# Optimization experiments

Hardware: AMD Instinct MI355X
Metric: run time of the kernel (lower is better)

Reference implementation:

```python
import jax, jax.numpy as jnp
import numpy as np

N, E = 50000, 400000          # nodes, edges
IN, H, OUT = 256, 512, 256    # channels
L, K = 2, 2                   # num_layers, Chebyshev order


def setup_inputs() -> dict:
    key = jax.random.key(0)
    ks = jax.random.split(key, 8)
    x = jax.random.normal(ks[0], (N, IN), jnp.float32)
    edge_index = jax.random.randint(ks[1], (2, E), 0, N)
    in_w = jax.random.normal(ks[2], (IN, H), jnp.float32) / np.float32(np.sqrt(IN))
    in_b = jnp.zeros((H,), jnp.float32)
    # ChebConv has K bias-free Linear layers per conv plus one bias vector
    conv_w = jax.random.normal(ks[3], (L, K, H, H), jnp.float32) / np.float32(np.sqrt(H))
    conv_b = jnp.zeros((L, H), jnp.float32)
    out_w = jax.random.normal(ks[4], (H, OUT), jnp.float32) / np.float32(np.sqrt(H))
    out_b = jnp.zeros((OUT,), jnp.float32)
    return dict(x=x, edge_index=edge_index, in_w=in_w, in_b=in_b,
                conv_w=conv_w, conv_b=conv_b, out_w=out_w, out_b=out_b)


def reference(x, edge_index, in_w, in_b, conv_w, conv_b, out_w, out_b):
    # PyG ChebConv normalization with lambda_max=2 (default):
    #   L_hat = 2/lambda_max * (I - D^{-1/2} A D^{-1/2}) - I = -D^{-1/2} A D^{-1/2}
    # i.e. off-diagonal weights -dinv[row]*w*dinv[col], diagonal 0.
    row, col = edge_index[0], edge_index[1]
    w = jnp.ones((E,), x.dtype)
    deg = jax.ops.segment_sum(w, row, num_segments=N)
    dinv = jnp.where(deg > 0, jax.lax.rsqrt(jnp.maximum(deg, 1e-12)), 0.0).astype(x.dtype)
    norm = -dinv[row] * w * dinv[col]  # [E]

    def prop(h):  # L_hat @ h  (gather from source row, scatter-add to target col)
        return jax.ops.segment_sum(norm[:, None] * h[row], col, num_segments=N)

    # dropout is identity in eval mode; reference is deterministic (eval)
    h = jax.nn.silu(x @ in_w + in_b)
    for l in range(L):
        # Chebyshev recursion, K=2: out = Tx0 @ W0 + (L_hat Tx0) @ W1 + b
        Tx0 = h
        out = Tx0 @ conv_w[l, 0]
        Tx1 = prop(Tx0)
        out = out + Tx1 @ conv_w[l, 1] + conv_b[l]
        h = jax.nn.silu(out)
    return h @ out_w + out_b
```

## Files before the change

kernel.cpp:

```cpp
#include <hip/hip_runtime.h>

#define H512 512

typedef short bf16x8 __attribute__((ext_vector_type(8)));
typedef float f32x4  __attribute__((ext_vector_type(4)));

__device__ __forceinline__ float silu_f(float v) { return v / (1.0f + __expf(-v)); }

__device__ __forceinline__ short f2bf(float f) {
    unsigned u = __float_as_uint(f);
    u = (u + 0x7FFFu + ((u >> 16) & 1u)) >> 16;
    return (short)u;
}
__device__ __forceinline__ float bf2f(short s) {
    return __uint_as_float(((unsigned)(unsigned short)s) << 16);
}


__global__ void hist_kernel(const int* __restrict__ row, const int* __restrict__ col,
                            float* __restrict__ deg, int* __restrict__ cnt, int E) {
    int e = blockIdx.x * blockDim.x + threadIdx.x;
    if (e < E) {
        atomicAdd(&deg[row[e]], 1.0f);
        atomicAdd(&cnt[col[e]], 1);
    }
}

__global__ void dinv_kernel(const float* __restrict__ deg, float* __restrict__ dinv, int n) {
    int i = blockIdx.x * blockDim.x + threadIdx.x;
    if (i < n) {
        float d = deg[i];
        dinv[i] = d > 0.0f ? rsqrtf(fmaxf(d, 1e-12f)) : 0.0f;
    }
}


__global__ __launch_bounds__(256) void bsum_kernel(const int* __restrict__ cnt,
                                                   int* __restrict__ bsum, int n) {
    __shared__ int s[4];
    int i = blockIdx.x * 256 + threadIdx.x;
    int v = (i < n) ? cnt[i] : 0;
    #pragma unroll
    for (int off = 32; off; off >>= 1) v += __shfl_down(v, off, 64);
    if ((threadIdx.x & 63) == 0) s[threadIdx.x >> 6] = v;
    __syncthreads();
    if (threadIdx.x == 0) bsum[blockIdx.x] = s[0] + s[1] + s[2] + s[3];
}

__global__ __launch_bounds__(256) void bscan_kernel(const int* __restrict__ bsum,
                                                    int* __restrict__ boff, int B) {
    __shared__ int s[256];
    int tid = threadIdx.x;
    int v = (tid < B) ? bsum[tid] : 0;
    s[tid] = v;
    __syncthreads();
    #pragma unroll
    for (int off = 1; off < 256; off <<= 1) {
        int t = (tid >= off) ? s[tid - off] : 0;
        __syncthreads();
        s[tid] += t;
        __syncthreads();
    }
    if (tid < B) boff[tid] = s[tid] - v;
}

__global__ __launch_bounds__(256) void cscan_kernel(const int* __restrict__ cnt,
                                                    const int* __restrict__ boff,
                                                    int* __restrict__ ptr,
                                                    int* __restrict__ ptr2, int n, int B) {
    __shared__ int s[256];
    int b = blockIdx.x, tid = threadIdx.x;
    int i = b * 256 + tid;
    int v = (i < n) ? cnt[i] : 0;
    s[tid] = v;
    __syncthreads();
    #pragma unroll
    for (int off = 1; off < 256; off <<= 1) {
        int t = (tid >= off) ? s[tid - off] : 0;
        __syncthreads();
        s[tid] += t;
        __syncthreads();
    }
    int exc = boff[b] + s[tid] - v;
    if (i < n) { ptr[i] = exc; ptr2[i] = exc; }
    if (b == B - 1 && tid == 255) ptr[n] = exc + v;
}

__global__ void scatter_kernel(const int* __restrict__ row, const int* __restrict__ col,
                               const float* __restrict__ dinv, int* __restrict__ ptr2,
                               int* __restrict__ esrc, float* __restrict__ ew, int E) {
    int e = blockIdx.x * blockDim.x + threadIdx.x;
    if (e >= E) return;
    int r = row[e], c = col[e];
    int pos = atomicAdd(&ptr2[c], 1);
    esrc[pos] = r;
    ew[pos]   = -dinv[r] * dinv[c];
}


__global__ void wt_kernel(const float* __restrict__ W, short* __restrict__ Wt, int K, int Nw) {
    int tid = blockIdx.x * blockDim.x + threadIdx.x;
    if (tid >= K * Nw) return;
    int n = tid / K, k = tid - n * K;
    Wt[(size_t)n * K + k] = f2bf(W[(size_t)k * Nw + n]);
}

__global__ void xconv_kernel(const float* __restrict__ x, short* __restrict__ xb,
                             int Nreal, int Mpad) {
    int tid = blockIdx.x * blockDim.x + threadIdx.x;
    if (tid >= Mpad * 32) return;
    int r = tid >> 5, c8 = (tid & 31) * 8;
    bf16x8 o = {0, 0, 0, 0, 0, 0, 0, 0};
    if (r < Nreal) {
        const float4 f0 = *(const float4*)(x + (size_t)r * 256 + c8);
        const float4 f1 = *(const float4*)(x + (size_t)r * 256 + c8 + 4);
        o[0] = f2bf(f0.x); o[1] = f2bf(f0.y); o[2] = f2bf(f0.z); o[3] = f2bf(f0.w);
        o[4] = f2bf(f1.x); o[5] = f2bf(f1.y); o[6] = f2bf(f1.z); o[7] = f2bf(f1.w);
    }
    *(bf16x8*)(xb + (size_t)r * 256 + c8) = o;
}


__global__ __launch_bounds__(256) void gather_kernel(
    const int* __restrict__ ptr, const int* __restrict__ esrc,
    const float* __restrict__ ew, const short* __restrict__ T,
    short* __restrict__ U, int N_)
{
    int t = threadIdx.x;
    int node = blockIdx.x * 4 + (t >> 6);
    if (node >= N_) return;
    int q = (t & 63) * 8;
    float acc[8] = {0.f, 0.f, 0.f, 0.f, 0.f, 0.f, 0.f, 0.f};
    const int i1 = ptr[node + 1];
    for (int i = ptr[node]; i < i1; ++i) {
        int s   = esrc[i];
        float w = ew[i];
        bf16x8 tv = *(const bf16x8*)(T + (size_t)s * H512 + q);
        #pragma unroll
        for (int j = 0; j < 8; ++j) acc[j] += w * bf2f(tv[j]);
    }
    bf16x8 o;
    #pragma unroll
    for (int j = 0; j < 8; ++j) o[j] = f2bf(acc[j]);
    *(bf16x8*)(U + (size_t)node * H512 + q) = o;
}


template<int ACCUM, int BIAS, int SILU, int F32OUT>
__global__ __launch_bounds__(256) void mfma_gemm(
    const short* __restrict__ A, int lda,
    const short* __restrict__ Bt, int ldb,
    const short* __restrict__ Cin, void* __restrict__ Cout, int ldc,
    const float* __restrict__ bias, int Mreal, int K)
{
    __shared__ alignas(16) short As[128 * 64];
    __shared__ alignas(16) short Bs[128 * 64];

    const int t    = threadIdx.x;
    const int lane = t & 63;
    const int wid  = t >> 6;
    const int m0   = blockIdx.y * 128;
    const int n0   = blockIdx.x * 128;
    const int wm   = wid >> 1;
    const int wn   = wid & 1;

    const int srow  = lane >> 3;
    const int scol  = (lane & 7) * 16;
    const int corig = scol ^ (srow << 4);
    const int cel   = corig >> 1;

    f32x4 acc[4][4];
    #pragma unroll
    for (int m = 0; m < 4; ++m)
        #pragma unroll
        for (int n = 0; n < 4; ++n)
            acc[m][n] = (f32x4){0.f, 0.f, 0.f, 0.f};

    const int r = lane & 15;
    const int g = lane >> 4;

    for (int k0 = 0; k0 < K; k0 += 64) {
        #pragma unroll
        for (int i = 0; i < 4; ++i) {
            const int r0 = (wid * 4 + i) * 8;
            const short* ga = A  + (size_t)(m0 + r0 + srow) * lda + (k0 + cel);
            __builtin_amdgcn_global_load_lds(
                (const __attribute__((address_space(1))) void*)ga,
                (__attribute__((address_space(3))) void*)(As + r0 * 64), 16, 0, 0);
            const short* gb = Bt + (size_t)(n0 + r0 + srow) * ldb + (k0 + cel);
            __builtin_amdgcn_global_load_lds(
                (const __attribute__((address_space(1))) void*)gb,
                (__attribute__((address_space(3))) void*)(Bs + r0 * 64), 16, 0, 0);
        }
        asm volatile("s_waitcnt vmcnt(0)" ::: "memory");
        __syncthreads();

        #pragma unroll
        for (int ks = 0; ks < 2; ++ks) {
            bf16x8 af[4], bfr[4];
            #pragma unroll
            for (int m = 0; m < 4; ++m) {
                const int rowA = wm * 64 + m * 16 + r;
                const int cb   = (ks * 64 + g * 16) ^ ((rowA & 7) << 4);
                af[m] = *(const bf16x8*)((const char*)As + rowA * 128 + cb);
            }
            #pragma unroll
            for (int n = 0; n < 4; ++n) {
                const int rowB = wn * 64 + n * 16 + r;
                const int cb   = (ks * 64 + g * 16) ^ ((rowB & 7) << 4);
                bfr[n] = *(const bf16x8*)((const char*)Bs + rowB * 128 + cb);
            }
            #pragma unroll
            for (int m = 0; m < 4; ++m)
                #pragma unroll
                for (int n = 0; n < 4; ++n)
                    acc[m][n] = __builtin_amdgcn_mfma_f32_16x16x32_bf16(
                        af[m], bfr[n], acc[m][n], 0, 0, 0);
        }
        __syncthreads();
    }

    #pragma unroll
    for (int n = 0; n < 4; ++n) {
        const int col = n0 + wn * 64 + n * 16 + r;
        float bb = 0.f;
        if (BIAS) bb = bias[col];
        #pragma unroll
        for (int m = 0; m < 4; ++m) {
            const int row0 = m0 + wm * 64 + m * 16 + g * 4;
            #pragma unroll
            for (int j = 0; j < 4; ++j) {
                const int rr = row0 + j;
                float v = acc[m][n][j];
                if (ACCUM) v += bf2f(Cin[(size_t)rr * ldc + col]);
                if (BIAS)  v += bb;
                if (SILU)  v = silu_f(v);
                if (F32OUT) {
                    if (rr < Mreal) ((float*)Cout)[(size_t)rr * ldc + col] = v;
                } else {
                    ((short*)Cout)[(size_t)rr * ldc + col] = f2bf(v);
                }
            }
        }
    }
}


extern "C" void kernel_launch(void* const* d_in, const int* in_sizes, int n_in,
                              void* d_out, int out_size, void* d_ws, size_t ws_size,
                              hipStream_t stream)
{
    const float* x      = (const float*)d_in[0];
    const int*   ei     = (const int*)  d_in[1];
    const float* in_w   = (const float*)d_in[2];
    const float* in_b   = (const float*)d_in[3];
    const float* conv_w = (const float*)d_in[4];
    const float* conv_b = (const float*)d_in[5];
    const float* out_w  = (const float*)d_in[6];
    const float* out_b  = (const float*)d_in[7];

    const int N = in_sizes[0] / 256;
    const int E = in_sizes[1] / 2;
    const int MPAD = ((N + 127) / 128) * 128;
    const int* row = ei;
    const int* col = ei + E;

    char* p = (char*)d_ws;
    short* h0 = (short*)p; p += (size_t)MPAD * H512 * 2;
    short* h1 = (short*)p; p += (size_t)MPAD * H512 * 2;
    short* T  = (short*)p; p += (size_t)MPAD * H512 * 2;
    short* U  = (short*)p; p += (size_t)MPAD * H512 * 2;
    short* xb = T;
    short* wti = (short*)p; p += (size_t)512 * 256 * 2;
    short* wtc = (short*)p; p += (size_t)4 * 512 * 512 * 2;
    short* wto = (short*)p; p += (size_t)256 * 512 * 2;
    float* deg  = (float*)p; p += (size_t)N * 4;
    float* dinv = (float*)p; p += (size_t)N * 4;
    float* ew   = (float*)p; p += (size_t)E * 4;
    int*   cnt  = (int*)p;   p += (size_t)N * 4;
    int*   ptr  = (int*)p;   p += (size_t)(N + 4) * 4;
    int*   ptr2 = (int*)p;   p += (size_t)N * 4;
    int*   esrc = (int*)p;   p += (size_t)E * 4;
    int*   bsum = (int*)p;   p += (size_t)256 * 4;
    int*   boff = (int*)p;   p += (size_t)256 * 4;

    const int NB = (N + 255) / 256;

    hipMemsetAsync(deg, 0, (size_t)N * sizeof(float), stream);
    hipMemsetAsync(cnt, 0, (size_t)N * sizeof(int), stream);
    hist_kernel<<<(E + 255) / 256, 256, 0, stream>>>(row, col, deg, cnt, E);
    dinv_kernel<<<(N + 255) / 256, 256, 0, stream>>>(deg, dinv, N);
    bsum_kernel <<<NB, 256, 0, stream>>>(cnt, bsum, N);
    bscan_kernel<<<1, 256, 0, stream>>>(bsum, boff, NB);
    cscan_kernel<<<NB, 256, 0, stream>>>(cnt, boff, ptr, ptr2, N, NB);
    scatter_kernel<<<(E + 255) / 256, 256, 0, stream>>>(row, col, dinv, ptr2, esrc, ew, E);

    wt_kernel<<<(256 * 512 + 255) / 256, 256, 0, stream>>>(in_w, wti, 256, 512);
    for (int i = 0; i < 4; ++i)
        wt_kernel<<<(512 * 512 + 255) / 256, 256, 0, stream>>>(
            conv_w + (size_t)i * 512 * 512, wtc + (size_t)i * 512 * 512, 512, 512);
    wt_kernel<<<(512 * 256 + 255) / 256, 256, 0, stream>>>(out_w, wto, 512, 256);
    xconv_kernel<<<(MPAD * 32 + 255) / 256, 256, 0, stream>>>(x, xb, N, MPAD);

    const int mt = MPAD / 128;

    mfma_gemm<0, 1, 1, 0><<<dim3(4, mt), 256, 0, stream>>>(
        xb, 256, wti, 256, nullptr, h0, H512, in_b, N, 256);

    short* hc = h0;
    short* hn = h1;
    for (int l = 0; l < 2; ++l) {
        mfma_gemm<0, 0, 0, 0><<<dim3(4, mt), 256, 0, stream>>>(
            hc, H512, wtc + (size_t)(l * 2 + 1) * 512 * 512, 512,
            nullptr, T, H512, nullptr, N, 512);
        gather_kernel<<<(N + 3) / 4, 256, 0, stream>>>(ptr, esrc, ew, T, U, N);
        mfma_gemm<1, 1, 1, 0><<<dim3(4, mt), 256, 0, stream>>>(
            hc, H512, wtc + (size_t)(l * 2 + 0) * 512 * 512, 512,
            U, hn, H512, conv_b + (size_t)l * H512, N, 512);
        short* tmp = hc; hc = hn; hn = tmp;
    }

    mfma_gemm<0, 1, 0, 1><<<dim3(2, mt), 256, 0, stream>>>(
        hc, H512, wto, 512, nullptr, d_out, 256, out_b, N, 512);
}
```

Measured before the change: 542.7 us.

## Stage GEMM epilogue through LDS for vectorized stores, swizzle blocks across XCDs

The GEMM epilogue now writes accumulators into a rotated LDS tile, then each thread handles a contiguous 32-column row segment. This lets Cin reads, bias loads and output stores use 16-byte vector accesses instead of scattered scalar ones. Workgroups are launched on a 1D grid and remapped so that neighbouring tiles land on the same XCD, aiming for better L2 reuse of the A and B panels. The weight transpose kernel also switches to an LDS-tiled, coalesced version. The cost is extra LDS traffic and two additional barriers per epilogue.

After: 576.2 us. 1.06x slower.

```diff
diff --git a/kernel.cpp b/kernel.cpp
--- a/kernel.cpp
+++ b/kernel.cpp
@@ -14,6 +14,14 @@
 }
 __device__ __forceinline__ float bf2f(short s) {
     return __uint_as_float(((unsigned)(unsigned short)s) << 16);
+}
+
+__device__ __forceinline__ int xcd_swz(int b, int nwg) {
+    const int NX = 8;
+    int q = nwg / NX, rr = nwg % NX;
+    int xcd = b % NX, idx = b / NX;
+    int base = (xcd < rr) ? xcd * (q + 1) : rr * (q + 1) + (xcd - rr) * q;
+    return base + idx;
 }
 
 
@@ -98,11 +106,25 @@
 }
 
 
-__global__ void wt_kernel(const float* __restrict__ W, short* __restrict__ Wt, int K, int Nw) {
-    int tid = blockIdx.x * blockDim.x + threadIdx.x;
-    if (tid >= K * Nw) return;
-    int n = tid / K, k = tid - n * K;
-    Wt[(size_t)n * K + k] = f2bf(W[(size_t)k * Nw + n]);
+__global__ __launch_bounds__(256) void wt_kernel(const float* __restrict__ W,
+                                                 short* __restrict__ Wt, int K, int Nw) {
+    __shared__ float tile[32][33];
+    const int tx = threadIdx.x & 31;
+    const int ty = threadIdx.x >> 5;
+    const int nt = Nw / 32;
+    const int k0 = (blockIdx.x / nt) * 32;
+    const int n0 = (blockIdx.x % nt) * 32;
+    #pragma unroll
+    for (int i = 0; i < 4; ++i) {
+        const int k = ty + i * 8;
+        tile[k][tx] = W[(size_t)(k0 + k) * Nw + n0 + tx];
+    }
+    __syncthreads();
+    #pragma unroll
+    for (int i = 0; i < 4; ++i) {
+        const int a = ty + i * 8;
+        Wt[(size_t)(n0 + a) * K + k0 + tx] = f2bf(tile[tx][a]);
+    }
 }
 
 __global__ void xconv_kernel(const float* __restrict__ x, short* __restrict__ xb,
@@ -151,16 +173,20 @@
     const short* __restrict__ A, int lda,
     const short* __restrict__ Bt, int ldb,
     const short* __restrict__ Cin, void* __restrict__ Cout, int ldc,
-    const float* __restrict__ bias, int Mreal, int K)
+    const float* __restrict__ bias, int Mreal, int K, int gx)
 {
-    __shared__ alignas(16) short As[128 * 64];
-    __shared__ alignas(16) short Bs[128 * 64];
+    __shared__ alignas(16) short lds[2 * 128 * 64];
+    short* As = lds;
+    short* Bs = lds + 128 * 64;
 
     const int t    = threadIdx.x;
     const int lane = t & 63;
     const int wid  = t >> 6;
-    const int m0   = blockIdx.y * 128;
-    const int n0   = blockIdx.x * 128;
+
+    const int wg = xcd_swz(blockIdx.x, gridDim.x);
+    const int m0 = (wg / gx) * 128;
+    const int n0 = (wg % gx) * 128;
+
     const int wm   = wid >> 1;
     const int wn   = wid & 1;
 
@@ -220,28 +246,77 @@
         __syncthreads();
     }
 
-    #pragma unroll
-    for (int n = 0; n < 4; ++n) {
-        const int col = n0 + wn * 64 + n * 16 + r;
-        float bb = 0.f;
-        if (BIAS) bb = bias[col];
-        #pragma unroll
-        for (int m = 0; m < 4; ++m) {
-            const int row0 = m0 + wm * 64 + m * 16 + g * 4;
+    float* fs = (float*)lds;
+    const int rrow = t >> 1;
+    const int hh   = (t & 1) * 32;
+    const int gr   = m0 + rrow;
+    const int rsft = (rrow & 15) << 2;
+
+    #pragma unroll
+    for (int p = 0; p < 2; ++p) {
+        if (wn == p) {
             #pragma unroll
-            for (int j = 0; j < 4; ++j) {
-                const int rr = row0 + j;
-                float v = acc[m][n][j];
-                if (ACCUM) v += bf2f(Cin[(size_t)rr * ldc + col]);
-                if (BIAS)  v += bb;
-                if (SILU)  v = silu_f(v);
-                if (F32OUT) {
-                    if (rr < Mreal) ((float*)Cout)[(size_t)rr * ldc + col] = v;
-                } else {
-                    ((short*)Cout)[(size_t)rr * ldc + col] = f2bf(v);
+            for (int m = 0; m < 4; ++m) {
+                #pragma unroll
+                for (int j = 0; j < 4; ++j) {
+                    const int row = wm * 64 + m * 16 + g * 4 + j;
+                    const int sft = (row & 15) << 2;
+                    #pragma unroll
+                    for (int n = 0; n < 4; ++n) {
+                        const int cl = (n * 16 + r + sft) & 63;
+                        fs[row * 64 + cl] = acc[m][n][j];
+                    }
                 }
             }
         }
+        __syncthreads();
+
+        {
+            const int gcb = n0 + p * 64 + hh;
+            float vv[32];
+            #pragma unroll
+            for (int c4 = 0; c4 < 8; ++c4) {
+                const int cl = (hh + c4 * 4 + rsft) & 63;
+                *(f32x4*)&vv[c4 * 4] = *(const f32x4*)&fs[rrow * 64 + cl];
+            }
+            if (ACCUM) {
+                #pragma unroll
+                for (int c8 = 0; c8 < 4; ++c8) {
+                    bf16x8 ci = *(const bf16x8*)(Cin + (size_t)gr * ldc + gcb + c8 * 8);
+                    #pragma unroll
+                    for (int j = 0; j < 8; ++j) vv[c8 * 8 + j] += bf2f(ci[j]);
+                }
+            }
+            if (BIAS) {
+                #pragma unroll
+                for (int c4 = 0; c4 < 8; ++c4) {
+                    const float4 bv = *(const float4*)(bias + gcb + c4 * 4);
+                    vv[c4 * 4 + 0] += bv.x; vv[c4 * 4 + 1] += bv.y;
+                    vv[c4 * 4 + 2] += bv.z; vv[c4 * 4 + 3] += bv.w;
+                }
+            }
+            if (SILU) {
+                #pragma unroll
+                for (int j = 0; j < 32; ++j) vv[j] = silu_f(vv[j]);
+            }
+            if (F32OUT) {
+                if (gr < Mreal) {
+                    #pragma unroll
+                    for (int c4 = 0; c4 < 8; ++c4)
+                        *(float4*)((float*)Cout + (size_t)gr * ldc + gcb + c4 * 4) =
+                            make_float4(vv[c4*4+0], vv[c4*4+1], vv[c4*4+2], vv[c4*4+3]);
+                }
+            } else {
+                #pragma unroll
+                for (int c8 = 0; c8 < 4; ++c8) {
+                    bf16x8 o;
+                    #pragma unroll
+                    for (int j = 0; j < 8; ++j) o[j] = f2bf(vv[c8 * 8 + j]);
+                    *(bf16x8*)((short*)Cout + (size_t)gr * ldc + gcb + c8 * 8) = o;
+                }
+            }
+        }
+        __syncthreads();
     }
 }
 
@@ -295,31 +370,31 @@
     cscan_kernel<<<NB, 256, 0, stream>>>(cnt, boff, ptr, ptr2, N, NB);
     scatter_kernel<<<(E + 255) / 256, 256, 0, stream>>>(row, col, dinv, ptr2, esrc, ew, E);
 
-    wt_kernel<<<(256 * 512 + 255) / 256, 256, 0, stream>>>(in_w, wti, 256, 512);
+    wt_kernel<<<(256 / 32) * (512 / 32), 256, 0, stream>>>(in_w, wti, 256, 512);
     for (int i = 0; i < 4; ++i)
-        wt_kernel<<<(512 * 512 + 255) / 256, 256, 0, stream>>>(
+        wt_kernel<<<(512 / 32) * (512 / 32), 256, 0, stream>>>(
             conv_w + (size_t)i * 512 * 512, wtc + (size_t)i * 512 * 512, 512, 512);
-    wt_kernel<<<(512 * 256 + 255) / 256, 256, 0, stream>>>(out_w, wto, 512, 256);
+    wt_kernel<<<(512 / 32) * (256 / 32), 256, 0, stream>>>(out_w, wto, 512, 256);
     xconv_kernel<<<(MPAD * 32 + 255) / 256, 256, 0, stream>>>(x, xb, N, MPAD);
 
     const int mt = MPAD / 128;
 
-    mfma_gemm<0, 1, 1, 0><<<dim3(4, mt), 256, 0, stream>>>(
-        xb, 256, wti, 256, nullptr, h0, H512, in_b, N, 256);
+    mfma_gemm<0, 1, 1, 0><<<dim3(4 * mt), 256, 0, stream>>>(
+        xb, 256, wti, 256, nullptr, h0, H512, in_b, N, 256, 4);
 
     short* hc = h0;
     short* hn = h1;
     for (int l = 0; l < 2; ++l) {
-        mfma_gemm<0, 0, 0, 0><<<dim3(4, mt), 256, 0, stream>>>(
+        mfma_gemm<0, 0, 0, 0><<<dim3(4 * mt), 256, 0, stream>>>(
             hc, H512, wtc + (size_t)(l * 2 + 1) * 512 * 512, 512,
-            nullptr, T, H512, nullptr, N, 512);
+            nullptr, T, H512, nullptr, N, 512, 4);
         gather_kernel<<<(N + 3) / 4, 256, 0, stream>>>(ptr, esrc, ew, T, U, N);
-        mfma_gemm<1, 1, 1, 0><<<dim3(4, mt), 256, 0, stream>>>(
+        mfma_gemm<1, 1, 1, 0><<<dim3(4 * mt), 256, 0, stream>>>(
             hc, H512, wtc + (size_t)(l * 2 + 0) * 512 * 512, 512,
-            U, hn, H512, conv_b + (size_t)l * H512, N, 512);
+            U, hn, H512, conv_b + (size_t)l * H512, N, 512, 4);
         short* tmp = hc; hc = hn; hn = tmp;
     }
 
-    mfma_gemm<0, 1, 0, 1><<<dim3(2, mt), 256, 0, stream>>>(
-        hc, H512, wto, 512, nullptr, d_out, 256, out_b, N, 512);
-}
+    mfma_gemm<0, 1, 0, 1><<<dim3(2 * mt), 256, 0, stream>>>(
+        hc, H512, wto, 512, nullptr, d_out, 256, out_b, N, 512, 2);
+}
```
